# Kernel optimization log

Hardware: AMD Instinct MI355X
Metric: run time of the kernel (lower is better)

## Reference

```python
import jax, jax.numpy as jnp
import numpy as np


def setup_inputs() -> dict:
    key = jax.random.key(0)
    ks = jax.random.split(key, 6)
    N, E, F_IN, H, C = 100000, 800000, 96, 128, 64
    x = jax.random.normal(ks[0], (N, F_IN), dtype=jnp.float32)
    W1 = jax.random.normal(ks[1], (F_IN, H), dtype=jnp.float32) * (1.0 / np.sqrt(F_IN))
    b1 = jnp.zeros((H,), dtype=jnp.float32)
    W2 = jax.random.normal(ks[2], (H, C), dtype=jnp.float32) * (1.0 / np.sqrt(H))
    b2 = jnp.zeros((C,), dtype=jnp.float32)
    edge_index = jax.random.randint(ks[3], (2, E), 0, N, dtype=jnp.int64)
    return {"x": x, "W1": W1, "b1": b1, "W2": W2, "b2": b2, "edge_index": edge_index}


def _gcn_norm(edge_index, num_nodes):
    # Add self-loops, compute symmetric normalization D^-1/2 (A+I) D^-1/2.
    loops = jnp.arange(num_nodes, dtype=edge_index.dtype)
    src = jnp.concatenate([edge_index[0], loops])
    dst = jnp.concatenate([edge_index[1], loops])
    deg = jax.ops.segment_sum(jnp.ones_like(dst, dtype=jnp.float32), dst,
                              num_segments=num_nodes)
    dinv = jnp.where(deg > 0, jax.lax.rsqrt(deg), 0.0)
    norm = dinv[src] * dinv[dst]  # [E+N]
    return src, dst, norm


def _gcn_conv(h, W, b, src, dst, norm, num_nodes):
    h = h @ W                              # [N, out] dense GEMM first (PyG order)
    msg = h[src] * norm[:, None]           # gather + scale, [E+N, out]
    agg = jax.ops.segment_sum(msg, dst, num_segments=num_nodes)
    return agg + b


def reference(x, W1, b1, W2, b2, edge_index):
    N = x.shape[0]
    src, dst, norm = _gcn_norm(edge_index, N)
    h = jax.nn.relu(_gcn_conv(x, W1, b1, src, dst, norm, N))
    embedding = h  # post-ReLU, pre-dropout (dropout inactive at eval)
    out = _gcn_conv(h, W2, b2, src, dst, norm, N)
    return jax.nn.log_softmax(out, axis=1), embedding
```

## Files before the change

### kernel.cpp

```cpp
#include <hip/hip_runtime.h>
#include <hip/hip_bf16.h>

#define NN 100000
#define NE 800000
#define FIN 96
#define FH 128
#define FC 64

#define BLOW 9
#define NBK 196
#define BCAP 5120
#define P1E 4096

typedef unsigned short u16;
typedef unsigned int u32;
typedef __attribute__((ext_vector_type(8))) __bf16 bf16x8;
typedef __attribute__((ext_vector_type(4))) float f32x4;

__device__ __forceinline__ float bf2f(u16 u) {
    u32 x = ((u32)u) << 16;
    return __builtin_bit_cast(float, x);
}
__device__ __forceinline__ u16 f2bf(float f) {
    u32 u = __builtin_bit_cast(u32, f);
    u += 0x7fffu + ((u >> 16) & 1u);
    return (u16)(u >> 16);
}
__device__ __forceinline__ void load8f(const u16* p, float* o) {
    uint4 pk = *(const uint4*)p;
    o[0] = bf2f((u16)pk.x); o[1] = bf2f((u16)(pk.x >> 16));
    o[2] = bf2f((u16)pk.y); o[3] = bf2f((u16)(pk.y >> 16));
    o[4] = bf2f((u16)pk.z); o[5] = bf2f((u16)(pk.z >> 16));
    o[6] = bf2f((u16)pk.w); o[7] = bf2f((u16)(pk.w >> 16));
}
__device__ __forceinline__ void store8bf(u16* p, const float* v) {
    uint4 pk;
    pk.x = (u32)f2bf(v[0]) | ((u32)f2bf(v[1]) << 16);
    pk.y = (u32)f2bf(v[2]) | ((u32)f2bf(v[3]) << 16);
    pk.z = (u32)f2bf(v[4]) | ((u32)f2bf(v[5]) << 16);
    pk.w = (u32)f2bf(v[6]) | ((u32)f2bf(v[7]) << 16);
    *(uint4*)p = pk;
}

__global__ __launch_bounds__(256) void k_bin(const int* __restrict__ srcs,
                                             const int* __restrict__ dsts,
                                             int* __restrict__ bucket_cursor,
                                             u32* __restrict__ bucket_data) {
    __shared__ int s_hist[256];
    __shared__ int s_base[256];
    __shared__ int s_cur[256];
    __shared__ int s_gbase[256];
    __shared__ u32 s_sorted[P1E];
    __shared__ unsigned char s_bkt[P1E];
    int t = threadIdx.x;
    int e0 = blockIdx.x * P1E;
    int n = NE - e0; if (n > P1E) n = P1E;
    s_hist[t] = 0;
    __syncthreads();
    u32 rp[16]; int rb[16];
#pragma unroll
    for (int j = 0; j < 16; j++) {
        int i = j * 256 + t;
        rb[j] = -1;
        if (i < n) {
            int s = srcs[e0 + i], d = dsts[e0 + i];
            int b = d >> BLOW;
            rb[j] = b;
            rp[j] = ((u32)(d & ((1 << BLOW) - 1)) << 17) | (u32)s;
            atomicAdd(&s_hist[b], 1);
        }
    }
    __syncthreads();
    int ct = s_hist[t];
    s_base[t] = ct;
    __syncthreads();
    for (int off = 1; off < 256; off <<= 1) {
        int v = (t >= off) ? s_base[t - off] : 0;
        __syncthreads();
        s_base[t] += v;
        __syncthreads();
    }
    int excl = s_base[t] - ct;
    __syncthreads();
    s_base[t] = excl;
    s_cur[t] = excl;
    if (t < NBK) s_gbase[t] = (ct > 0) ? atomicAdd(&bucket_cursor[t], ct) : 0;
    __syncthreads();
#pragma unroll
    for (int j = 0; j < 16; j++) {
        if (rb[j] >= 0) {
            int r = atomicAdd(&s_cur[rb[j]], 1);
            s_sorted[r] = rp[j];
            s_bkt[r] = (unsigned char)rb[j];
        }
    }
    __syncthreads();
    for (int i = t; i < n; i += 256) {
        int b = s_bkt[i];
        int gpos = s_gbase[b] + (i - s_base[b]);
        if (gpos < BCAP)
            bucket_data[(size_t)b * BCAP + gpos] = s_sorted[i];
    }
}

__global__ __launch_bounds__(256) void k_csr(const int* __restrict__ bucket_cursor,
                                             const u32* __restrict__ bucket_data,
                                             int* __restrict__ row_start,
                                             float* __restrict__ dinv,
                                             int* __restrict__ src_sorted) {
    __shared__ int s_c[256];
    __shared__ int s_cnt[512];
    __shared__ int s_ps[256];
    __shared__ int s_off[512];
    __shared__ int s_cur[512];
    __shared__ u32 s_edges[BCAP];
    int t = threadIdx.x;
    int b = blockIdx.x;
    int nbe = bucket_cursor[b];
    if (nbe > BCAP) nbe = BCAP;
    s_c[t] = (t < NBK) ? bucket_cursor[t] : 0;
    __syncthreads();
    for (int off = 1; off < 256; off <<= 1) {
        int v = (t >= off) ? s_c[t - off] : 0;
        __syncthreads();
        s_c[t] += v;
        __syncthreads();
    }
    int bbase = s_c[b] - nbe;
    s_cnt[t] = 0; s_cnt[t + 256] = 0;
    __syncthreads();
    for (int i = t; i < nbe; i += 256) {
        u32 p = bucket_data[(size_t)b * BCAP + i];
        s_edges[i] = p;
        atomicAdd(&s_cnt[p >> 17], 1);
    }
    __syncthreads();
    int c0 = s_cnt[2 * t], c1 = s_cnt[2 * t + 1];
    s_ps[t] = c0 + c1;
    __syncthreads();
    for (int off = 1; off < 256; off <<= 1) {
        int v = (t >= off) ? s_ps[t - off] : 0;
        __syncthreads();
        s_ps[t] += v;
        __syncthreads();
    }
    int pexcl = s_ps[t] - (c0 + c1);
    s_off[2 * t] = pexcl;      s_cur[2 * t] = pexcl;
    s_off[2 * t + 1] = pexcl + c0; s_cur[2 * t + 1] = pexcl + c0;
    __syncthreads();
#pragma unroll
    for (int k = 0; k < 2; k++) {
        int ld = k * 256 + t;
        int gd = b * 512 + ld;
        if (gd < NN) {
            row_start[gd] = bbase + s_off[ld];
            dinv[gd] = rsqrtf((float)s_cnt[ld] + 1.0f);
        }
    }
    if (b == 0 && t == 0) row_start[NN] = NE;
    for (int i = t; i < nbe; i += 256) {
        u32 p = s_edges[i];
        int d = p >> 17;
        int r = atomicAdd(&s_cur[d], 1);
        src_sorted[bbase + r] = (int)(p & 0x1FFFFu);
    }
}

__global__ void k_cvt_x(const float* __restrict__ x, u16* __restrict__ xb) {
    int i = (blockIdx.x * 256 + threadIdx.x) * 4;
    if (i < NN * FIN) {
        float4 f = *(const float4*)(x + i);
        ushort4 o = {f2bf(f.x), f2bf(f.y), f2bf(f.z), f2bf(f.w)};
        *(ushort4*)(xb + i) = o;
    }
}
__global__ void k_cvt_w1(const float* __restrict__ W1, u16* __restrict__ W1t) {
    int i = blockIdx.x * 256 + threadIdx.x;
    if (i < FH * FIN) {
        int n = i / FIN, k = i % FIN;
        W1t[i] = f2bf(W1[k * FH + n]);
    }
}
__global__ void k_cvt_w2(const float* __restrict__ W2, u16* __restrict__ W2t) {
    int i = blockIdx.x * 256 + threadIdx.x;
    if (i < FC * FH) {
        int n = i / FH, k = i % FH;
        W2t[i] = f2bf(W2[k * FC + n]);
    }
}

__global__ void k_agg1(const u16* __restrict__ xb, const float* __restrict__ dinv,
                       const int* __restrict__ row_start, const int* __restrict__ src_sorted,
                       u16* __restrict__ aggx) {
    int tid = blockIdx.x * 256 + threadIdx.x;
    int dst = tid / 12, q = tid % 12;
    if (dst >= NN) return;
    int rs = row_start[dst], re = row_start[dst + 1];
    float dv = dinv[dst];
    float acc[8], v[8];
    load8f(xb + (size_t)dst * FIN + q * 8, acc);
#pragma unroll
    for (int j = 0; j < 8; j++) acc[j] *= dv;
    for (int e = rs; e < re; e++) {
        int s = src_sorted[e];
        float ds_ = dinv[s];
        load8f(xb + (size_t)s * FIN + q * 8, v);
#pragma unroll
        for (int j = 0; j < 8; j++) acc[j] += v[j] * ds_;
    }
#pragma unroll
    for (int j = 0; j < 8; j++) acc[j] *= dv;
    store8bf(aggx + (size_t)dst * FIN + q * 8, acc);
}

__global__ void k_agg2(const u16* __restrict__ zb, const float* __restrict__ dinv,
                       const int* __restrict__ row_start, const int* __restrict__ src_sorted,
                       const float* __restrict__ b2, float* __restrict__ logits) {
    int tid = blockIdx.x * 256 + threadIdx.x;
    int dst = tid / 8, q = tid % 8;
    if (dst >= NN) return;
    int rs = row_start[dst], re = row_start[dst + 1];
    float dv = dinv[dst];
    float acc[8], v[8];
    load8f(zb + (size_t)dst * FC + q * 8, acc);
#pragma unroll
    for (int j = 0; j < 8; j++) acc[j] *= dv;
    for (int e = rs; e < re; e++) {
        int s = src_sorted[e];
        float ds_ = dinv[s];
        load8f(zb + (size_t)s * FC + q * 8, v);
#pragma unroll
        for (int j = 0; j < 8; j++) acc[j] += v[j] * ds_;
    }
    float r[8];
#pragma unroll
    for (int j = 0; j < 8; j++) r[j] = acc[j] * dv + b2[q * 8 + j];
    float4 o0 = {r[0], r[1], r[2], r[3]}, o1 = {r[4], r[5], r[6], r[7]};
    *(float4*)(logits + (size_t)dst * FC + q * 8) = o0;
    *(float4*)(logits + (size_t)dst * FC + q * 8 + 4) = o1;
}

__global__ __launch_bounds__(256) void k_gemm1(const u16* __restrict__ aggx,
                                               const u16* __restrict__ W1t,
                                               const float* __restrict__ b1,
                                               float* __restrict__ h, u16* __restrict__ hb) {
    int wave = blockIdx.x * 4 + (threadIdx.x >> 6);
    int row0 = wave << 4;
    if (row0 >= NN) return;
    int lane = threadIdx.x & 63;
    int m = lane & 15, quad = lane >> 4;
    f32x4 acc[8] = {{0,0,0,0},{0,0,0,0},{0,0,0,0},{0,0,0,0},
                    {0,0,0,0},{0,0,0,0},{0,0,0,0},{0,0,0,0}};
#pragma unroll
    for (int kt = 0; kt < 3; kt++) {
        bf16x8 a = *(const bf16x8*)(const void*)(aggx + (size_t)(row0 + m) * FIN + kt * 32 + quad * 8);
#pragma unroll
        for (int nt = 0; nt < 8; nt++) {
            bf16x8 b = *(const bf16x8*)(const void*)(W1t + (size_t)(nt * 16 + m) * FIN + kt * 32 + quad * 8);
            acc[nt] = __builtin_amdgcn_mfma_f32_16x16x32_bf16(a, b, acc[nt], 0, 0, 0);
        }
    }
#pragma unroll
    for (int nt = 0; nt < 8; nt++) {
        int c = nt * 16 + m;
        float bias = b1[c];
#pragma unroll
        for (int i = 0; i < 4; i++) {
            int r = row0 + quad * 4 + i;
            float val = acc[nt][i] + bias;
            val = val > 0.0f ? val : 0.0f;
            h[(size_t)r * FH + c] = val;
            hb[(size_t)r * FH + c] = f2bf(val);
        }
    }
}

__global__ __launch_bounds__(256) void k_gemm2(const u16* __restrict__ hb,
                                               const u16* __restrict__ W2t,
                                               u16* __restrict__ zb) {
    int wave = blockIdx.x * 4 + (threadIdx.x >> 6);
    int row0 = wave << 4;
    if (row0 >= NN) return;
    int lane = threadIdx.x & 63;
    int m = lane & 15, quad = lane >> 4;
    f32x4 acc[4] = {{0,0,0,0},{0,0,0,0},{0,0,0,0},{0,0,0,0}};
#pragma unroll
    for (int kt = 0; kt < 4; kt++) {
        bf16x8 a = *(const bf16x8*)(const void*)(hb + (size_t)(row0 + m) * FH + kt * 32 + quad * 8);
#pragma unroll
        for (int nt = 0; nt < 4; nt++) {
            bf16x8 b = *(const bf16x8*)(const void*)(W2t + (size_t)(nt * 16 + m) * FH + kt * 32 + quad * 8);
            acc[nt] = __builtin_amdgcn_mfma_f32_16x16x32_bf16(a, b, acc[nt], 0, 0, 0);
        }
    }
#pragma unroll
    for (int nt = 0; nt < 4; nt++) {
        int c = nt * 16 + m;
#pragma unroll
        for (int i = 0; i < 4; i++) {
            int r = row0 + quad * 4 + i;
            zb[(size_t)r * FC + c] = f2bf(acc[nt][i]);
        }
    }
}

__global__ void k_lsm(float* __restrict__ logits) {
    int row = blockIdx.x * 4 + (threadIdx.x >> 6);
    if (row >= NN) return;
    int lane = threadIdx.x & 63;
    float v = logits[(size_t)row * FC + lane];
    float mx = v;
#pragma unroll
    for (int d = 32; d; d >>= 1) mx = fmaxf(mx, __shfl_xor(mx, d, 64));
    float e = expf(v - mx);
    float s = e;
#pragma unroll
    for (int d = 32; d; d >>= 1) s += __shfl_xor(s, d, 64);
    logits[(size_t)row * FC + lane] = v - mx - logf(s);
}

extern "C" void kernel_launch(void* const* d_in, const int* in_sizes, int n_in,
                              void* d_out, int out_size, void* d_ws, size_t ws_size,
                              hipStream_t stream) {
    const float* x  = (const float*)d_in[0];
    const float* W1 = (const float*)d_in[1];
    const float* b1 = (const float*)d_in[2];
    const float* W2 = (const float*)d_in[3];
    const float* b2 = (const float*)d_in[4];
    const int* ei   = (const int*)d_in[5];
    const int* srcs = ei;
    const int* dsts = ei + NE;

    float* logits = (float*)d_out;
    float* emb    = (float*)d_out + (size_t)NN * FC;

    char* w = (char*)d_ws;
    float* dinv       = (float*)w; w += 400000;
    int*   row_start  = (int*)w;   w += 400128;
    int*   src_sorted = (int*)w;   w += 3200000;
    int*   bucket_cursor = (int*)w; w += 1024;
    u16*   xb         = (u16*)w;   w += 19200000;
    u16*   aggx       = (u16*)w;   w += 19200000;
    u16*   W1t        = (u16*)w;   w += 24576;
    u16*   W2t        = (u16*)w;   w += 16384;
    u16*   hb         = (u16*)w;   w += 25600000;
    u16*   zb         = (u16*)w;   w += 12800000;
    u32*   bucket_data = (u32*)aggx;

    hipMemsetAsync(bucket_cursor, 0, NBK * 4, stream);
    k_bin<<<(NE + P1E - 1) / P1E, 256, 0, stream>>>(srcs, dsts, bucket_cursor, bucket_data);
    k_csr<<<NBK, 256, 0, stream>>>(bucket_cursor, bucket_data, row_start, dinv, src_sorted);
    k_cvt_x<<<(NN * FIN / 4 + 255) / 256, 256, 0, stream>>>(x, xb);
    k_cvt_w1<<<(FH * FIN + 255) / 256, 256, 0, stream>>>(W1, W1t);
    k_cvt_w2<<<(FC * FH + 255) / 256, 256, 0, stream>>>(W2, W2t);
    k_agg1<<<(NN * 12 + 255) / 256, 256, 0, stream>>>(xb, dinv, row_start, src_sorted, aggx);
    k_gemm1<<<(NN / 16 + 3) / 4, 256, 0, stream>>>(aggx, W1t, b1, emb, hb);
    k_gemm2<<<(NN / 16 + 3) / 4, 256, 0, stream>>>(hb, W2t, zb);
    k_agg2<<<(NN * 8 + 255) / 256, 256, 0, stream>>>(zb, dinv, row_start, src_sorted, b2, logits);
    k_lsm<<<(NN + 3) / 4, 256, 0, stream>>>(logits);
}
```

Measured before the change: 266.6 us.

## Fuse GEMM1+GEMM2 via LDS tile and aggregation2 with log-softmax

```diff
diff --git a/kernel.cpp b/kernel.cpp
--- a/kernel.cpp
+++ b/kernel.cpp
@@ -145,7 +145,7 @@
         __syncthreads();
     }
     int pexcl = s_ps[t] - (c0 + c1);
-    s_off[2 * t] = pexcl;      s_cur[2 * t] = pexcl;
+    s_off[2 * t] = pexcl;          s_cur[2 * t] = pexcl;
     s_off[2 * t + 1] = pexcl + c0; s_cur[2 * t + 1] = pexcl + c0;
     __syncthreads();
 #pragma unroll
@@ -174,18 +174,16 @@
         *(ushort4*)(xb + i) = o;
     }
 }
-__global__ void k_cvt_w1(const float* __restrict__ W1, u16* __restrict__ W1t) {
+__global__ void k_cvt_w(const float* __restrict__ W1, const float* __restrict__ W2,
+                        u16* __restrict__ W1t, u16* __restrict__ W2t) {
     int i = blockIdx.x * 256 + threadIdx.x;
     if (i < FH * FIN) {
         int n = i / FIN, k = i % FIN;
         W1t[i] = f2bf(W1[k * FH + n]);
-    }
-}
-__global__ void k_cvt_w2(const float* __restrict__ W2, u16* __restrict__ W2t) {
-    int i = blockIdx.x * 256 + threadIdx.x;
-    if (i < FC * FH) {
-        int n = i / FH, k = i % FH;
-        W2t[i] = f2bf(W2[k * FC + n]);
+    } else if (i < FH * FIN + FC * FH) {
+        int j = i - FH * FIN;
+        int n = j / FH, k = j % FH;
+        W2t[j] = f2bf(W2[k * FC + n]);
     }
 }
 
@@ -197,126 +195,120 @@
     if (dst >= NN) return;
     int rs = row_start[dst], re = row_start[dst + 1];
     float dv = dinv[dst];
-    float acc[8], v[8];
+    float acc[8], v0[8], v1[8];
     load8f(xb + (size_t)dst * FIN + q * 8, acc);
 #pragma unroll
     for (int j = 0; j < 8; j++) acc[j] *= dv;
-    for (int e = rs; e < re; e++) {
-        int s = src_sorted[e];
-        float ds_ = dinv[s];
-        load8f(xb + (size_t)s * FIN + q * 8, v);
-#pragma unroll
-        for (int j = 0; j < 8; j++) acc[j] += v[j] * ds_;
+    int e = rs;
+    for (; e + 1 < re; e += 2) {
+        int s0 = src_sorted[e], s1 = src_sorted[e + 1];
+        float d0 = dinv[s0], d1 = dinv[s1];
+        load8f(xb + (size_t)s0 * FIN + q * 8, v0);
+        load8f(xb + (size_t)s1 * FIN + q * 8, v1);
+#pragma unroll
+        for (int j = 0; j < 8; j++) acc[j] += v0[j] * d0 + v1[j] * d1;
+    }
+    if (e < re) {
+        int s0 = src_sorted[e];
+        float d0 = dinv[s0];
+        load8f(xb + (size_t)s0 * FIN + q * 8, v0);
+#pragma unroll
+        for (int j = 0; j < 8; j++) acc[j] += v0[j] * d0;
     }
 #pragma unroll
     for (int j = 0; j < 8; j++) acc[j] *= dv;
     store8bf(aggx + (size_t)dst * FIN + q * 8, acc);
 }
 
-__global__ void k_agg2(const u16* __restrict__ zb, const float* __restrict__ dinv,
-                       const int* __restrict__ row_start, const int* __restrict__ src_sorted,
-                       const float* __restrict__ b2, float* __restrict__ logits) {
-    int tid = blockIdx.x * 256 + threadIdx.x;
-    int dst = tid / 8, q = tid % 8;
+#define LDSW 136
+__global__ __launch_bounds__(128) void k_gemm12(const u16* __restrict__ aggx,
+                                                const u16* __restrict__ W1t,
+                                                const float* __restrict__ b1,
+                                                const u16* __restrict__ W2t,
+                                                float* __restrict__ emb,
+                                                u16* __restrict__ zb) {
+    __shared__ u16 sh[2][16 * LDSW];
+    int wid = threadIdx.x >> 6, lane = threadIdx.x & 63;
+    int wave = blockIdx.x * 2 + wid;
+    int row0 = wave << 4;
+    int m = lane & 15, quad = lane >> 4;
+    f32x4 acc[8] = {{0,0,0,0},{0,0,0,0},{0,0,0,0},{0,0,0,0},
+                    {0,0,0,0},{0,0,0,0},{0,0,0,0},{0,0,0,0}};
+#pragma unroll
+    for (int kt = 0; kt < 3; kt++) {
+        bf16x8 a = *(const bf16x8*)(const void*)(aggx + (size_t)(row0 + m) * FIN + kt * 32 + quad * 8);
+#pragma unroll
+        for (int nt = 0; nt < 8; nt++) {
+            bf16x8 b = *(const bf16x8*)(const void*)(W1t + (size_t)(nt * 16 + m) * FIN + kt * 32 + quad * 8);
+            acc[nt] = __builtin_amdgcn_mfma_f32_16x16x32_bf16(a, b, acc[nt], 0, 0, 0);
+        }
+    }
+    u16* tile = sh[wid];
+#pragma unroll
+    for (int nt = 0; nt < 8; nt++) {
+        int c = nt * 16 + m;
+        float bias = b1[c];
+#pragma unroll
+        for (int i = 0; i < 4; i++) {
+            int r = quad * 4 + i;
+            float val = acc[nt][i] + bias;
+            val = val > 0.0f ? val : 0.0f;
+            emb[(size_t)(row0 + r) * FH + c] = val;
+            tile[r * LDSW + c] = f2bf(val);
+        }
+    }
+    __syncthreads();
+    f32x4 zacc[4] = {{0,0,0,0},{0,0,0,0},{0,0,0,0},{0,0,0,0}};
+#pragma unroll
+    for (int kt = 0; kt < 4; kt++) {
+        bf16x8 a = *(const bf16x8*)(const void*)(tile + m * LDSW + kt * 32 + quad * 8);
+#pragma unroll
+        for (int nt = 0; nt < 4; nt++) {
+            bf16x8 b = *(const bf16x8*)(const void*)(W2t + (size_t)(nt * 16 + m) * FH + kt * 32 + quad * 8);
+            zacc[nt] = __builtin_amdgcn_mfma_f32_16x16x32_bf16(a, b, zacc[nt], 0, 0, 0);
+        }
+    }
+#pragma unroll
+    for (int nt = 0; nt < 4; nt++) {
+        int c = nt * 16 + m;
+#pragma unroll
+        for (int i = 0; i < 4; i++) {
+            int r = row0 + quad * 4 + i;
+            zb[(size_t)r * FC + c] = f2bf(zacc[nt][i]);
+        }
+    }
+}
+
+__global__ void k_agg2lsm(const u16* __restrict__ zb, const float* __restrict__ dinv,
+                          const int* __restrict__ row_start, const int* __restrict__ src_sorted,
+                          const float* __restrict__ b2, float* __restrict__ logits) {
+    int wid = threadIdx.x >> 6, lane = threadIdx.x & 63;
+    int dst = blockIdx.x * 4 + wid;
     if (dst >= NN) return;
     int rs = row_start[dst], re = row_start[dst + 1];
     float dv = dinv[dst];
-    float acc[8], v[8];
-    load8f(zb + (size_t)dst * FC + q * 8, acc);
-#pragma unroll
-    for (int j = 0; j < 8; j++) acc[j] *= dv;
-    for (int e = rs; e < re; e++) {
-        int s = src_sorted[e];
-        float ds_ = dinv[s];
-        load8f(zb + (size_t)s * FC + q * 8, v);
-#pragma unroll
-        for (int j = 0; j < 8; j++) acc[j] += v[j] * ds_;
-    }
-    float r[8];
-#pragma unroll
-    for (int j = 0; j < 8; j++) r[j] = acc[j] * dv + b2[q * 8 + j];
-    float4 o0 = {r[0], r[1], r[2], r[3]}, o1 = {r[4], r[5], r[6], r[7]};
-    *(float4*)(logits + (size_t)dst * FC + q * 8) = o0;
-    *(float4*)(logits + (size_t)dst * FC + q * 8 + 4) = o1;
-}
-
-__global__ __launch_bounds__(256) void k_gemm1(const u16* __restrict__ aggx,
-                                               const u16* __restrict__ W1t,
-                                               const float* __restrict__ b1,
-                                               float* __restrict__ h, u16* __restrict__ hb) {
-    int wave = blockIdx.x * 4 + (threadIdx.x >> 6);
-    int row0 = wave << 4;
-    if (row0 >= NN) return;
-    int lane = threadIdx.x & 63;
-    int m = lane & 15, quad = lane >> 4;
-    f32x4 acc[8] = {{0,0,0,0},{0,0,0,0},{0,0,0,0},{0,0,0,0},
-                    {0,0,0,0},{0,0,0,0},{0,0,0,0},{0,0,0,0}};
-#pragma unroll
-    for (int kt = 0; kt < 3; kt++) {
-        bf16x8 a = *(const bf16x8*)(const void*)(aggx + (size_t)(row0 + m) * FIN + kt * 32 + quad * 8);
-#pragma unroll
-        for (int nt = 0; nt < 8; nt++) {
-            bf16x8 b = *(const bf16x8*)(const void*)(W1t + (size_t)(nt * 16 + m) * FIN + kt * 32 + quad * 8);
-            acc[nt] = __builtin_amdgcn_mfma_f32_16x16x32_bf16(a, b, acc[nt], 0, 0, 0);
-        }
-    }
-#pragma unroll
-    for (int nt = 0; nt < 8; nt++) {
-        int c = nt * 16 + m;
-        float bias = b1[c];
-#pragma unroll
-        for (int i = 0; i < 4; i++) {
-            int r = row0 + quad * 4 + i;
-            float val = acc[nt][i] + bias;
-            val = val > 0.0f ? val : 0.0f;
-            h[(size_t)r * FH + c] = val;
-            hb[(size_t)r * FH + c] = f2bf(val);
-        }
-    }
-}
-
-__global__ __launch_bounds__(256) void k_gemm2(const u16* __restrict__ hb,
-                                               const u16* __restrict__ W2t,
-                                               u16* __restrict__ zb) {
-    int wave = blockIdx.x * 4 + (threadIdx.x >> 6);
-    int row0 = wave << 4;
-    if (row0 >= NN) return;
-    int lane = threadIdx.x & 63;
-    int m = lane & 15, quad = lane >> 4;
-    f32x4 acc[4] = {{0,0,0,0},{0,0,0,0},{0,0,0,0},{0,0,0,0}};
-#pragma unroll
-    for (int kt = 0; kt < 4; kt++) {
-        bf16x8 a = *(const bf16x8*)(const void*)(hb + (size_t)(row0 + m) * FH + kt * 32 + quad * 8);
-#pragma unroll
-        for (int nt = 0; nt < 4; nt++) {
-            bf16x8 b = *(const bf16x8*)(const void*)(W2t + (size_t)(nt * 16 + m) * FH + kt * 32 + quad * 8);
-            acc[nt] = __builtin_amdgcn_mfma_f32_16x16x32_bf16(a, b, acc[nt], 0, 0, 0);
-        }
-    }
-#pragma unroll
-    for (int nt = 0; nt < 4; nt++) {
-        int c = nt * 16 + m;
-#pragma unroll
-        for (int i = 0; i < 4; i++) {
-            int r = row0 + quad * 4 + i;
-            zb[(size_t)r * FC + c] = f2bf(acc[nt][i]);
-        }
-    }
-}
-
-__global__ void k_lsm(float* __restrict__ logits) {
-    int row = blockIdx.x * 4 + (threadIdx.x >> 6);
-    if (row >= NN) return;
-    int lane = threadIdx.x & 63;
-    float v = logits[(size_t)row * FC + lane];
+    float acc = bf2f(zb[(size_t)dst * FC + lane]) * dv;
+    int e = rs;
+    for (; e + 1 < re; e += 2) {
+        int s0 = src_sorted[e], s1 = src_sorted[e + 1];
+        float d0 = dinv[s0], d1 = dinv[s1];
+        float v0 = bf2f(zb[(size_t)s0 * FC + lane]);
+        float v1 = bf2f(zb[(size_t)s1 * FC + lane]);
+        acc += v0 * d0 + v1 * d1;
+    }
+    if (e < re) {
+        int s0 = src_sorted[e];
+        acc += bf2f(zb[(size_t)s0 * FC + lane]) * dinv[s0];
+    }
+    float v = acc * dv + b2[lane];
     float mx = v;
 #pragma unroll
     for (int d = 32; d; d >>= 1) mx = fmaxf(mx, __shfl_xor(mx, d, 64));
-    float e = expf(v - mx);
-    float s = e;
+    float ex = expf(v - mx);
+    float s = ex;
 #pragma unroll
     for (int d = 32; d; d >>= 1) s += __shfl_xor(s, d, 64);
-    logits[(size_t)row * FC + lane] = v - mx - logf(s);
+    logits[(size_t)dst * FC + lane] = v - mx - logf(s);
 }
 
 extern "C" void kernel_launch(void* const* d_in, const int* in_sizes, int n_in,
@@ -343,7 +335,6 @@
     u16*   aggx       = (u16*)w;   w += 19200000;
     u16*   W1t        = (u16*)w;   w += 24576;
     u16*   W2t        = (u16*)w;   w += 16384;
-    u16*   hb         = (u16*)w;   w += 25600000;
     u16*   zb         = (u16*)w;   w += 12800000;
     u32*   bucket_data = (u32*)aggx;
 
@@ -351,11 +342,8 @@
     k_bin<<<(NE + P1E - 1) / P1E, 256, 0, stream>>>(srcs, dsts, bucket_cursor, bucket_data);
     k_csr<<<NBK, 256, 0, stream>>>(bucket_cursor, bucket_data, row_start, dinv, src_sorted);
     k_cvt_x<<<(NN * FIN / 4 + 255) / 256, 256, 0, stream>>>(x, xb);
-    k_cvt_w1<<<(FH * FIN + 255) / 256, 256, 0, stream>>>(W1, W1t);
-    k_cvt_w2<<<(FC * FH + 255) / 256, 256, 0, stream>>>(W2, W2t);
+    k_cvt_w<<<(FH * FIN + FC * FH + 255) / 256, 256, 0, stream>>>(W1, W2, W1t, W2t);
     k_agg1<<<(NN * 12 + 255) / 256, 256, 0, stream>>>(xb, dinv, row_start, src_sorted, aggx);
-    k_gemm1<<<(NN / 16 + 3) / 4, 256, 0, stream>>>(aggx, W1t, b1, emb, hb);
-    k_gemm2<<<(NN / 16 + 3) / 4, 256, 0, stream>>>(hb, W2t, zb);
-    k_agg2<<<(NN * 8 + 255) / 256, 256, 0, stream>>>(zb, dinv, row_start, src_sorted, b2, logits);
-    k_lsm<<<(NN + 3) / 4, 256, 0, stream>>>(logits);
-}
+    k_gemm12<<<NN / 32, 128, 0, stream>>>(aggx, W1t, b1, W2t, emb, zb);
+    k_agg2lsm<<<(NN + 3) / 4, 256, 0, stream>>>(zb, dinv, row_start, src_sorted, b2, logits);
+}
```

Measured after the change: 262.7 us. About the same (-1.5%).
